# Kernel tuning notes

Hardware: AMD Instinct MI355X
Metric: run time of the kernel (lower is better)

The kernel has to match this reference:

```python
import jax, jax.numpy as jnp
import numpy as np

N_NODES = 100000
N_EDGES = 1600000
F_IN, HID, N_CLS = 128, 64, 40


def gcn_conv(x, src, dst, W, b, n_nodes):
    # x: [N, Fin] -> [N, Fout]; edges already include self-loops.
    h = x @ W  # [N, Fout]
    ones = jnp.ones_like(src, dtype=h.dtype)
    deg = jax.ops.segment_sum(ones, dst, num_segments=n_nodes)  # [N]
    dinv = jnp.where(deg > 0, jax.lax.rsqrt(deg), 0.0)
    norm = dinv[src] * dinv[dst]  # [E]
    msg = h[src] * norm[:, None]  # gather + scale
    out = jax.ops.segment_sum(msg, dst, num_segments=n_nodes)  # scatter-sum
    return out + b


def setup_inputs() -> dict:
    key = jax.random.key(0)
    ks = jax.random.split(key, 8)
    x = jax.random.normal(ks[0], (N_NODES, F_IN), dtype=jnp.float32)
    edge_index = jax.random.randint(ks[1], (2, N_EDGES), 0, N_NODES, dtype=jnp.int64)

    def glorot(k, fi, fo):
        s = float(np.sqrt(6.0 / (fi + fo)))
        return jax.random.uniform(k, (fi, fo), jnp.float32, -s, s)

    return {
        "x": x,
        "edge_index": edge_index,
        "W1": glorot(ks[2], F_IN, HID), "b1": jnp.zeros((HID,), jnp.float32),
        "W2": glorot(ks[3], HID, HID), "b2": jnp.zeros((HID,), jnp.float32),
        "W3": glorot(ks[4], HID, N_CLS), "b3": jnp.zeros((N_CLS,), jnp.float32),
    }


def reference(x, edge_index, W1, b1, W2, b2, W3, b3):
    n = x.shape[0]
    loop = jnp.arange(n, dtype=edge_index.dtype)
    src = jnp.concatenate([edge_index[0], loop])  # add self-loops
    dst = jnp.concatenate([edge_index[1], loop])
    # layer 1..3: GCNConv -> relu -> dropout(eval: identity)
    h = jax.nn.relu(gcn_conv(x, src, dst, W1, b1, n))
    h = jax.nn.relu(gcn_conv(h, src, dst, W2, b2, n))
    h = jax.nn.relu(gcn_conv(h, src, dst, W3, b3, n))
    return jax.nn.log_softmax(h, axis=1)
```

## Files before the change

### kernel.cpp

```cpp
#include <hip/hip_runtime.h>
#include <math.h>

typedef _Float16 half8   __attribute__((ext_vector_type(8)));
typedef float    float4v __attribute__((ext_vector_type(4)));

#define CAP   6144
#define EPB   8192

static __device__ __forceinline__ unsigned short f32_to_f16u(float f) {
    _Float16 h = (_Float16)f;
    return __builtin_bit_cast(unsigned short, h);
}


static __device__ __forceinline__ void prep_body(
    const float* __restrict__ W, unsigned short* __restrict__ Wf, int K, int M)
{
    const int NT = (M + 15) >> 4, NTC = NT << 4, KS = K >> 5;
    for (int i = threadIdx.x; i < K * NTC; i += 256) {
        int k = i / NTC, nn = i - k * NTC;
        unsigned short hv = 0;
        if (nn < M) hv = f32_to_f16u(W[(size_t)k * M + nn]);
        int s = k >> 5, q = (k >> 3) & 3, j = k & 7;
        int u = nn >> 4, lane = (q << 4) | (nn & 15);
        Wf[((u * KS + s) << 9) + (lane << 3) + j] = hv;
    }
}

template<int KK, int NT, int STRIDE, int MOUT, bool INF32, bool SCALE>
static __device__ __forceinline__ void gemm_body(
    unsigned short* __restrict__ ldsA, const void* __restrict__ Xin,
    const unsigned short* __restrict__ Wf, const float* __restrict__ dinv,
    unsigned short* __restrict__ H, int n, int bid)
{
    constexpr int KS = KK >> 5;
    const int tid = threadIdx.x;
    const int n0  = bid * 64;
    const int wv   = tid >> 6;
    const int lane = tid & 63;

    half8 bf[NT * KS];
    #pragma unroll
    for (int u = 0; u < NT; ++u)
        #pragma unroll
        for (int s = 0; s < KS; ++s)
            bf[u * KS + s] = *(const half8*)&Wf[((u * KS + s) << 9) + (lane << 3)];

    {
        const int rl = tid >> 3;
        const int kl = tid & 7;
        #pragma unroll
        for (int rb = 0; rb < 64; rb += 32) {
            int r = rl + rb;
            int node = n0 + r;
            int t = r >> 4, m = r & 15;
            if (INF32) {
                #pragma unroll
                for (int kq8 = 0; kq8 < (KK >> 2); kq8 += 8) {
                    int k0 = (kl + kq8) << 2;
                    unsigned short h[4] = {0, 0, 0, 0};
                    if (node < n) {
                        const float* xp = (const float*)Xin + (size_t)node * KK + k0;
                        float4v v = *(const float4v*)xp;
                        #pragma unroll
                        for (int i = 0; i < 4; ++i) h[i] = f32_to_f16u(v[i]);
                    }
                    int s = k0 >> 5, q = (k0 >> 3) & 3, j0 = k0 & 7;
                    int lds_lane = (q << 4) | m;
                    unsigned short* p = &ldsA[((t * KS + s) << 9) + (lds_lane << 3) + j0];
                    *(uint2*)p = make_uint2((unsigned)h[0] | ((unsigned)h[1] << 16),
                                            (unsigned)h[2] | ((unsigned)h[3] << 16));
                }
            } else {
                uint4 v = make_uint4(0, 0, 0, 0);
                if (node < n)
                    v = *(const uint4*)((const unsigned short*)Xin + (size_t)node * KK + (kl << 3));
                int k0 = kl << 3;
                int s = k0 >> 5, q = (k0 >> 3) & 3;
                unsigned short* p = &ldsA[((t * KS + s) << 9) + ((((q << 4) | m)) << 3)];
                *(uint4*)p = v;
            }
        }
    }

    __syncthreads();

    float4v acc[NT];
    #pragma unroll
    for (int u = 0; u < NT; ++u) acc[u] = (float4v){0.f, 0.f, 0.f, 0.f};

    #pragma unroll
    for (int s = 0; s < KS; ++s) {
        half8 a = *(const half8*)&ldsA[((wv * KS + s) << 9) + (lane << 3)];
        #pragma unroll
        for (int u = 0; u < NT; ++u)
            acc[u] = __builtin_amdgcn_mfma_f32_16x16x32_f16(a, bf[u * KS + s], acc[u], 0, 0, 0);
    }

    const int mc = lane & 15;
    const int quad = lane >> 4;
    #pragma unroll
    for (int reg = 0; reg < 4; ++reg) {
        int node = n0 + (wv << 4) + (quad << 2) + reg;
        if (node >= n) continue;
        float dv = SCALE ? dinv[node] : 1.0f;
        #pragma unroll
        for (int u = 0; u < NT; ++u) {
            int col = (u << 4) + mc;
            if (col < MOUT)
                H[(size_t)node * STRIDE + col] = f32_to_f16u(SCALE ? acc[u][reg] * dv
                                                                   : acc[u][reg]);
        }
    }
}

struct CsrS {
    int cnt[256]; int sc[256]; int cur[256];
    unsigned int pin[CAP]; int pout[CAP];
};

static __device__ __forceinline__ void csr_body(
    CsrS& S, const unsigned int* __restrict__ bint, const int* __restrict__ bcur,
    int2* __restrict__ rp2, float* __restrict__ dinv, int* __restrict__ es,
    int n, int b)
{
    const int tid = threadIdx.x;
    int total = bcur[b]; if (total > CAP) total = CAP;
    const unsigned int* bp = bint + (size_t)b * CAP;
    int* ep = es + (size_t)b * CAP;
    const int base = b * CAP;

    S.cnt[tid] = 0;
    __syncthreads();
    for (int i = tid; i < total; i += 256) {
        unsigned int v = bp[i];
        S.pin[i] = v;
        atomicAdd(&S.cnt[v & 255], 1);
    }
    __syncthreads();

    int v = S.cnt[tid];
    S.sc[tid] = v;
    __syncthreads();
    for (int off = 1; off < 256; off <<= 1) {
        int x = (tid >= off) ? S.sc[tid - off] : 0;
        __syncthreads();
        S.sc[tid] += x;
        __syncthreads();
    }
    int excl = S.sc[tid] - v;
    int node = (b << 8) + tid;
    if (node < n) {
        rp2[node]  = make_int2(base + excl, base + excl + v);
        dinv[node] = rsqrtf((float)(v + 1));
    }
    S.cur[tid] = excl;
    __syncthreads();

    for (int i = tid; i < total; i += 256) {
        unsigned int p = S.pin[i];
        int r = atomicAdd(&S.cur[p & 255], 1);
        S.pout[r] = (int)(p >> 8);
    }
    __syncthreads();

    for (int i = tid; i < total; i += 256)
        ep[i] = S.pout[i];
}


__global__ __launch_bounds__(256) void bin_prep(
    const int* __restrict__ src, const int* __restrict__ dst,
    int* __restrict__ bcur, unsigned int* __restrict__ bint, int E, int NB, int EB,
    const float* __restrict__ W1, const float* __restrict__ W2, const float* __restrict__ W3,
    unsigned short* __restrict__ Wf1, unsigned short* __restrict__ Wf2,
    unsigned short* __restrict__ Wf3)
{
    __shared__ unsigned int pay[EPB];
    __shared__ unsigned int targ[EPB];
    __shared__ int h[512];
    __shared__ int h2[512];
    __shared__ int sc[512];
    __shared__ int rbase[512];

    const int bx = (int)blockIdx.x;
    if (bx >= EB) {
        int k = bx - EB;
        if (k == 0)      prep_body(W1, Wf1, 128, 64);
        else if (k == 1) prep_body(W2, Wf2, 64, 64);
        else             prep_body(W3, Wf3, 64, 40);
        return;
    }

    const int tid  = threadIdx.x;
    const int base = bx * EPB;
    int end = base + EPB; if (end > E) end = E;
    const int total = end - base;
    const int L4 = total & ~3;

    h[tid] = 0; h[tid + 256] = 0;
    h2[tid] = 0; h2[tid + 256] = 0;
    __syncthreads();

    for (int i = tid << 2; i < L4; i += 1024) {
        int4 d4 = *(const int4*)(dst + base + i);
        atomicAdd(&h[d4.x >> 8], 1);
        atomicAdd(&h[d4.y >> 8], 1);
        atomicAdd(&h[d4.z >> 8], 1);
        atomicAdd(&h[d4.w >> 8], 1);
    }
    for (int i = L4 + tid; i < total; i += 256)
        atomicAdd(&h[dst[base + i] >> 8], 1);
    __syncthreads();

    int v0 = h[tid], v1 = h[tid + 256];
    sc[tid] = v0; sc[tid + 256] = v1;
    __syncthreads();
    for (int off = 1; off < 512; off <<= 1) {
        int x0 = (tid >= off) ? sc[tid - off] : 0;
        int x1 = (tid + 256 >= off) ? sc[tid + 256 - off] : 0;
        __syncthreads();
        sc[tid] += x0; sc[tid + 256] += x1;
        __syncthreads();
    }

    for (int j = tid; j < NB; j += 256) {
        int c = h[j];
        rbase[j] = c ? atomicAdd(&bcur[j], c) : 0;
    }
    __syncthreads();

    {
        auto place = [&](int d, int s) {
            int bkt  = d >> 8;
            int rank = atomicAdd(&h2[bkt], 1);
            int loc  = sc[bkt] - h[bkt] + rank;
            pay[loc] = ((unsigned int)s << 8) | (unsigned int)(d & 255);
            unsigned int t = (unsigned int)(rbase[bkt] + rank);
            targ[loc] = (t < (unsigned int)CAP)
                      ? (unsigned int)bkt * CAP + t : 0xFFFFFFFFu;
        };
        for (int i = tid << 2; i < L4; i += 1024) {
            int4 d4 = *(const int4*)(dst + base + i);
            int4 s4 = *(const int4*)(src + base + i);
            place(d4.x, s4.x); place(d4.y, s4.y);
            place(d4.z, s4.z); place(d4.w, s4.w);
        }
        for (int i = L4 + tid; i < total; i += 256)
            place(dst[base + i], src[base + i]);
    }
    __syncthreads();

    for (int i = tid; i < total; i += 256) {
        unsigned int t = targ[i];
        if (t != 0xFFFFFFFFu) bint[t] = pay[i];
    }
}


union SmemU {
    CsrS csr;
    unsigned short ldsA[4 * 4 * 512];
};

__global__ __launch_bounds__(256) void csr_gemm1(
    const unsigned int* __restrict__ bint, const int* __restrict__ bcur,
    int2* __restrict__ rp2, float* __restrict__ dinv, int* __restrict__ es,
    const float* __restrict__ x, const unsigned short* __restrict__ Wf1,
    unsigned short* __restrict__ H1, int n, int NBb)
{
    __shared__ __align__(16) SmemU sm;
    const int bx = (int)blockIdx.x;
    if (bx < NBb)
        csr_body(sm.csr, bint, bcur, rp2, dinv, es, n, bx);
    else
        gemm_body<128, 4, 64, 64, true, false>(sm.ldsA, x, Wf1, nullptr, H1, n, bx - NBb);
}


template<int KK, int NT, int STRIDE, int MOUT>
__global__ __launch_bounds__(256) void gemm_t(
    const void* __restrict__ Xin, const unsigned short* __restrict__ Wf,
    const float* __restrict__ dinv, unsigned short* __restrict__ H, int n)
{
    constexpr int KS = KK >> 5;
    __shared__ __align__(16) unsigned short ldsA[4 * KS * 512];
    gemm_body<KK, NT, STRIDE, MOUT, false, true>(ldsA, Xin, Wf, dinv, H, n, blockIdx.x);
}


template<int MOUT, int ROWU4, bool SRCSCALE>
__global__ __launch_bounds__(256) void gather_t(
    const int2* __restrict__ rp2, const int* __restrict__ es,
    const unsigned short* __restrict__ H, const float* __restrict__ dinv,
    const float* __restrict__ bias, unsigned short* __restrict__ Aout, int n)
{
    const int lane   = threadIdx.x & 63;
    const int half   = lane >> 5;
    const int lane32 = lane & 31;
    const int slot   = (lane >> 3) & 3;
    const int c8     = lane & 7;
    const bool act   = c8 < ROWU4;
    const uint4* H4  = (const uint4*)H;

    float bi[8];
    #pragma unroll
    for (int i = 0; i < 8; ++i) bi[i] = bias[(c8 << 3) + i];

    const half8 hz = {(_Float16)0, (_Float16)0, (_Float16)0, (_Float16)0,
                      (_Float16)0, (_Float16)0, (_Float16)0, (_Float16)0};

    const int TW2 = (int)(gridDim.x << 3);
    for (int nb = (((int)blockIdx.x << 2) + ((int)threadIdx.x >> 6)) << 1; nb < n; nb += TW2) {
        const int node = nb + half;
        const int2 e = rp2[node];
        const float dv = dinv[node];

        half8 hacc = hz;
        half8 self = hz;
        if (slot == 0 && act) {
            self = __builtin_bit_cast(half8, H4[(size_t)node * ROWU4 + c8]);
            if (!SRCSCALE) hacc = self;
        }

        for (int cb = e.x; cb < e.y; cb += 32) {
            const int rem = e.y - cb;
            int eidx = cb + lane32; if (eidx > e.y - 1) eidx = e.y - 1;
            const int ei = es[eidx];
            #pragma unroll
            for (int j = 0; j < 8; ++j) {
                const int idx = (j << 2) + slot;
                const int s = __shfl(ei, (half << 5) + idx, 64);
                if (idx < rem && act) {
                    half8 row = __builtin_bit_cast(half8, H4[(size_t)s * ROWU4 + c8]);
                    if (SRCSCALE) {
                        _Float16 dh = (_Float16)dinv[s];
                        half8 ds = {dh, dh, dh, dh, dh, dh, dh, dh};
                        hacc = hacc + ds * row;
                    } else {
                        hacc = hacc + row;
                    }
                }
            }
        }

        #pragma unroll
        for (int step = 8; step <= 16; step <<= 1) {
            uint4 u = __builtin_bit_cast(uint4, hacc);
            uint4 o;
            o.x = __shfl_xor(u.x, step, 64);
            o.y = __shfl_xor(u.y, step, 64);
            o.z = __shfl_xor(u.z, step, 64);
            o.w = __shfl_xor(u.w, step, 64);
            hacc = hacc + __builtin_bit_cast(half8, o);
        }

        if (slot == 0) {
            unsigned short o[8];
            #pragma unroll
            for (int i = 0; i < 8; ++i) {
                float a = SRCSCALE ? ((float)hacc[i] + (float)self[i] * dv) * dv
                                   : (float)hacc[i] * dv;
                o[i] = f32_to_f16u(fmaxf(a + bi[i], 0.0f));
            }
            uint4 w;
            w.x = (unsigned int)o[0] | ((unsigned int)o[1] << 16);
            w.y = (unsigned int)o[2] | ((unsigned int)o[3] << 16);
            w.z = (unsigned int)o[4] | ((unsigned int)o[5] << 16);
            w.w = (unsigned int)o[6] | ((unsigned int)o[7] << 16);
            ((uint4*)Aout)[(size_t)node * 8 + c8] = w;
        }
    }
}


template<int MOUT, int ROWU4>
__global__ __launch_bounds__(256) void gather_softmax(
    const int2* __restrict__ rp2, const int* __restrict__ es,
    const unsigned short* __restrict__ H, const float* __restrict__ dinv,
    const float* __restrict__ bias, float* __restrict__ out, int n)
{
    const int lane   = threadIdx.x & 63;
    const int half   = lane >> 5;
    const int lane32 = lane & 31;
    const int slot   = (lane >> 3) & 3;
    const int c8     = lane & 7;
    const bool act   = c8 < ROWU4;
    const uint4* H4  = (const uint4*)H;

    float bi[8];
    #pragma unroll
    for (int i = 0; i < 8; ++i) {
        int col = (c8 << 3) + i;
        bi[i] = (col < MOUT) ? bias[col] : 0.0f;
    }

    const half8 hz = {(_Float16)0, (_Float16)0, (_Float16)0, (_Float16)0,
                      (_Float16)0, (_Float16)0, (_Float16)0, (_Float16)0};

    const int TW2 = (int)(gridDim.x << 3);
    for (int nb = (((int)blockIdx.x << 2) + ((int)threadIdx.x >> 6)) << 1; nb < n; nb += TW2) {
        const int node = nb + half;
        const int2 e = rp2[node];
        const float dv = dinv[node];

        half8 hacc = hz;
        if (slot == 0 && act)
            hacc = __builtin_bit_cast(half8, H4[(size_t)node * ROWU4 + c8]);

        for (int cb = e.x; cb < e.y; cb += 32) {
            const int rem = e.y - cb;
            int eidx = cb + lane32; if (eidx > e.y - 1) eidx = e.y - 1;
            const int ei = es[eidx];
            #pragma unroll
            for (int j = 0; j < 8; ++j) {
                const int idx = (j << 2) + slot;
                const int s = __shfl(ei, (half << 5) + idx, 64);
                if (idx < rem && act)
                    hacc = hacc + __builtin_bit_cast(half8, H4[(size_t)s * ROWU4 + c8]);
            }
        }

        #pragma unroll
        for (int step = 8; step <= 16; step <<= 1) {
            uint4 u = __builtin_bit_cast(uint4, hacc);
            uint4 o;
            o.x = __shfl_xor(u.x, step, 64);
            o.y = __shfl_xor(u.y, step, 64);
            o.z = __shfl_xor(u.z, step, 64);
            o.w = __shfl_xor(u.w, step, 64);
            hacc = hacc + __builtin_bit_cast(half8, o);
        }

        float z[8]; float m = -INFINITY;
        #pragma unroll
        for (int i = 0; i < 8; ++i) {
            int col = (c8 << 3) + i;
            z[i] = (col < MOUT && act) ? fmaxf((float)hacc[i] * dv + bi[i], 0.0f)
                                       : -INFINITY;
            m = fmaxf(m, z[i]);
        }
        m = fmaxf(m, __shfl_xor(m, 1, 64));
        m = fmaxf(m, __shfl_xor(m, 2, 64));
        m = fmaxf(m, __shfl_xor(m, 4, 64));
        float s = 0.0f;
        #pragma unroll
        for (int i = 0; i < 8; ++i) s += expf(z[i] - m);
        s += __shfl_xor(s, 1, 64);
        s += __shfl_xor(s, 2, 64);
        s += __shfl_xor(s, 4, 64);
        float ls = logf(s) + m;
        if (slot == 0 && c8 < (MOUT + 7) / 8) {
            float* op = out + (size_t)node * MOUT + (c8 << 3);
            float4v o0 = {z[0] - ls, z[1] - ls, z[2] - ls, z[3] - ls};
            float4v o1 = {z[4] - ls, z[5] - ls, z[6] - ls, z[7] - ls};
            *(float4v*)op = o0;
            *(float4v*)(op + 4) = o1;
        }
    }
}


extern "C" void kernel_launch(void* const* d_in, const int* in_sizes, int n_in,
                              void* d_out, int out_size, void* d_ws, size_t ws_size,
                              hipStream_t stream)
{
    const float* x  = (const float*)d_in[0];
    const int*   ei = (const int*)  d_in[1];
    const float* W1 = (const float*)d_in[2];
    const float* b1 = (const float*)d_in[3];
    const float* W2 = (const float*)d_in[4];
    const float* b2 = (const float*)d_in[5];
    const float* W3 = (const float*)d_in[6];
    const float* b3 = (const float*)d_in[7];

    const int F_IN = 128;
    const int n = in_sizes[0] / F_IN;
    const int E = in_sizes[1] / 2;
    const int* src = ei;
    const int* dst = ei + E;
    float* out = (float*)d_out;

    const int NB = (n + 255) >> 8;

    auto align = [](size_t v) { return (v + 255) & ~(size_t)255; };
    char* w = (char*)d_ws;
    size_t off = 0;
    float*          dinv = (float*)(w + off);          off = align(off + (size_t)n * 4);
    unsigned short* H1   = (unsigned short*)(w + off); off = align(off + (size_t)n * 64 * 2);
    unsigned short* A    = (unsigned short*)(w + off); off = align(off + (size_t)n * 64 * 2);
    unsigned short* H3   = (unsigned short*)(w + off); off = align(off + (size_t)n * 40 * 2);
    int2*           rp2  = (int2*)(w + off);           off = align(off + (size_t)n * 8);
    int*            es   = (int*)(w + off);            off = align(off + (size_t)NB * CAP * 4);
    unsigned int*   bint = (unsigned int*)(w + off);   off = align(off + (size_t)NB * CAP * 4);
    int*            bcur = (int*)(w + off);            off = align(off + (size_t)512 * 4);
    unsigned short* Wf1  = (unsigned short*)(w + off); off = align(off + (size_t)8192 * 2);
    unsigned short* Wf2  = (unsigned short*)(w + off); off = align(off + (size_t)4096 * 2);
    unsigned short* Wf3  = (unsigned short*)(w + off); off = align(off + (size_t)3072 * 2);
    unsigned short* H2   = H1;

    const int BLK = 256;
    auto cdiv = [](int a, int b) { return (a + b - 1) / b; };
    const int EB = cdiv(E, EPB);
    const int GB = cdiv(n, 64);
    const int GG = 2048;

    hipMemsetAsync(bcur, 0, (size_t)512 * 4, stream);
    bin_prep<<<EB + 3, BLK, 0, stream>>>(src, dst, bcur, bint, E, NB, EB,
                                         W1, W2, W3, Wf1, Wf2, Wf3);

    csr_gemm1<<<NB + GB, BLK, 0, stream>>>(bint, bcur, rp2, dinv, es, x, Wf1, H1, n, NB);

    gather_t<64, 8, true><<<GG, BLK, 0, stream>>>(rp2, es, H1, dinv, b1, A, n);

    gemm_t<64, 4, 64, 64><<<GB, BLK, 0, stream>>>(A, Wf2, dinv, H2, n);
    gather_t<64, 8, false><<<GG, BLK, 0, stream>>>(rp2, es, H2, dinv, b2, A, n);

    gemm_t<64, 3, 40, 40><<<GB, BLK, 0, stream>>>(A, Wf3, dinv, H3, n);
    gather_softmax<40, 5><<<GG, BLK, 0, stream>>>(rp2, es, H3, dinv, b3, out, n);
}
```

Measured before the change: 250.2 us.

## Widen CSR buckets to 512 nodes and halve edges per binning block

Node buckets for the two-pass CSR build grow from 256 to 512 destination nodes, which halves the bucket count and the per-bucket global atomics. Each binning block now handles 4096 edges instead of 8192, giving more blocks in flight. The CSR build no longer stages the input in shared memory and re-reads it from global on the second pass, so its LDS footprint shrinks. The risks are more CSR work per block (512 nodes, up to 9216 edges) and fewer CSR blocks. Packing 9 bits of destination leaves 23 bits for the source index, enough for 100k nodes.

```diff
diff --git a/kernel.cpp b/kernel.cpp
--- a/kernel.cpp
+++ b/kernel.cpp
@@ -4,8 +4,9 @@
 typedef _Float16 half8   __attribute__((ext_vector_type(8)));
 typedef float    float4v __attribute__((ext_vector_type(4)));
 
-#define CAP   6144
-#define EPB   8192
+#define NPB   512
+#define CAP   9216
+#define EPB   4096
 
 static __device__ __forceinline__ unsigned short f32_to_f16u(float f) {
     _Float16 h = (_Float16)f;
@@ -115,8 +116,8 @@
 }
 
 struct CsrS {
-    int cnt[256]; int sc[256]; int cur[256];
-    unsigned int pin[CAP]; int pout[CAP];
+    int cnt[512]; int sc[512]; int cur[512];
+    int pout[CAP];
 };
 
 static __device__ __forceinline__ void csr_body(
@@ -130,37 +131,43 @@
     int* ep = es + (size_t)b * CAP;
     const int base = b * CAP;
 
-    S.cnt[tid] = 0;
-    __syncthreads();
+    S.cnt[tid] = 0; S.cnt[tid + 256] = 0;
+    __syncthreads();
+    for (int i = tid; i < total; i += 256)
+        atomicAdd(&S.cnt[bp[i] & 511], 1);
+    __syncthreads();
+
+    int v0 = S.cnt[tid], v1 = S.cnt[tid + 256];
+    S.sc[tid] = v0; S.sc[tid + 256] = v1;
+    __syncthreads();
+    for (int off = 1; off < 512; off <<= 1) {
+        int x0 = (tid >= off) ? S.sc[tid - off] : 0;
+        int x1 = (tid + 256 >= off) ? S.sc[tid + 256 - off] : 0;
+        __syncthreads();
+        S.sc[tid] += x0; S.sc[tid + 256] += x1;
+        __syncthreads();
+    }
+    {
+        int excl0 = S.sc[tid] - v0;
+        int excl1 = S.sc[tid + 256] - v1;
+        int node0 = (b << 9) + tid;
+        int node1 = node0 + 256;
+        if (node0 < n) {
+            rp2[node0]  = make_int2(base + excl0, base + excl0 + v0);
+            dinv[node0] = rsqrtf((float)(v0 + 1));
+        }
+        if (node1 < n) {
+            rp2[node1]  = make_int2(base + excl1, base + excl1 + v1);
+            dinv[node1] = rsqrtf((float)(v1 + 1));
+        }
+        S.cur[tid] = excl0; S.cur[tid + 256] = excl1;
+    }
+    __syncthreads();
+
     for (int i = tid; i < total; i += 256) {
-        unsigned int v = bp[i];
-        S.pin[i] = v;
-        atomicAdd(&S.cnt[v & 255], 1);
-    }
-    __syncthreads();
-
-    int v = S.cnt[tid];
-    S.sc[tid] = v;
-    __syncthreads();
-    for (int off = 1; off < 256; off <<= 1) {
-        int x = (tid >= off) ? S.sc[tid - off] : 0;
-        __syncthreads();
-        S.sc[tid] += x;
-        __syncthreads();
-    }
-    int excl = S.sc[tid] - v;
-    int node = (b << 8) + tid;
-    if (node < n) {
-        rp2[node]  = make_int2(base + excl, base + excl + v);
-        dinv[node] = rsqrtf((float)(v + 1));
-    }
-    S.cur[tid] = excl;
-    __syncthreads();
-
-    for (int i = tid; i < total; i += 256) {
-        unsigned int p = S.pin[i];
-        int r = atomicAdd(&S.cur[p & 255], 1);
-        S.pout[r] = (int)(p >> 8);
+        unsigned int p = bp[i];
+        int r = atomicAdd(&S.cur[p & 511], 1);
+        S.pout[r] = (int)(p >> 9);
     }
     __syncthreads();
 
@@ -178,10 +185,10 @@
 {
     __shared__ unsigned int pay[EPB];
     __shared__ unsigned int targ[EPB];
-    __shared__ int h[512];
-    __shared__ int h2[512];
-    __shared__ int sc[512];
-    __shared__ int rbase[512];
+    __shared__ int h[256];
+    __shared__ int h2[256];
+    __shared__ int sc[256];
+    __shared__ int rbase[256];
 
     const int bx = (int)blockIdx.x;
     if (bx >= EB) {
@@ -198,44 +205,42 @@
     const int total = end - base;
     const int L4 = total & ~3;
 
-    h[tid] = 0; h[tid + 256] = 0;
-    h2[tid] = 0; h2[tid + 256] = 0;
+    h[tid] = 0; h2[tid] = 0;
     __syncthreads();
 
     for (int i = tid << 2; i < L4; i += 1024) {
         int4 d4 = *(const int4*)(dst + base + i);
-        atomicAdd(&h[d4.x >> 8], 1);
-        atomicAdd(&h[d4.y >> 8], 1);
-        atomicAdd(&h[d4.z >> 8], 1);
-        atomicAdd(&h[d4.w >> 8], 1);
+        atomicAdd(&h[d4.x >> 9], 1);
+        atomicAdd(&h[d4.y >> 9], 1);
+        atomicAdd(&h[d4.z >> 9], 1);
+        atomicAdd(&h[d4.w >> 9], 1);
     }
     for (int i = L4 + tid; i < total; i += 256)
-        atomicAdd(&h[dst[base + i] >> 8], 1);
-    __syncthreads();
-
-    int v0 = h[tid], v1 = h[tid + 256];
-    sc[tid] = v0; sc[tid + 256] = v1;
-    __syncthreads();
-    for (int off = 1; off < 512; off <<= 1) {
-        int x0 = (tid >= off) ? sc[tid - off] : 0;
-        int x1 = (tid + 256 >= off) ? sc[tid + 256 - off] : 0;
+        atomicAdd(&h[dst[base + i] >> 9], 1);
+    __syncthreads();
+
+    int v = h[tid];
+    sc[tid] = v;
+    __syncthreads();
+    for (int off = 1; off < 256; off <<= 1) {
+        int x = (tid >= off) ? sc[tid - off] : 0;
         __syncthreads();
-        sc[tid] += x0; sc[tid + 256] += x1;
+        sc[tid] += x;
         __syncthreads();
     }
 
-    for (int j = tid; j < NB; j += 256) {
-        int c = h[j];
-        rbase[j] = c ? atomicAdd(&bcur[j], c) : 0;
+    if (tid < NB) {
+        int c = h[tid];
+        rbase[tid] = c ? atomicAdd(&bcur[tid], c) : 0;
     }
     __syncthreads();
 
     {
         auto place = [&](int d, int s) {
-            int bkt  = d >> 8;
+            int bkt  = d >> 9;
             int rank = atomicAdd(&h2[bkt], 1);
             int loc  = sc[bkt] - h[bkt] + rank;
-            pay[loc] = ((unsigned int)s << 8) | (unsigned int)(d & 255);
+            pay[loc] = ((unsigned int)s << 9) | (unsigned int)(d & 511);
             unsigned int t = (unsigned int)(rbase[bkt] + rank);
             targ[loc] = (t < (unsigned int)CAP)
                       ? (unsigned int)bkt * CAP + t : 0xFFFFFFFFu;
@@ -481,7 +486,7 @@
     const int* dst = ei + E;
     float* out = (float*)d_out;
 
-    const int NB = (n + 255) >> 8;
+    const int NB = (n + NPB - 1) / NPB;
 
     auto align = [](size_t v) { return (v + 255) & ~(size_t)255; };
     char* w = (char*)d_ws;
```

Measured after the change: 255.6 us. 1.02x slower.

## Split gather/GEMM by node halves to overlap second-half gather with first-half GEMM

Applied to the files above, without the earlier changes.

Each gather+GEMM layer pair is split into node halves. A mixed kernel runs the gather for the second half of the nodes alongside the GEMM for the first half, whose gather finished in an earlier launch. A final GEMM launch then handles the remaining rows. This aims to fill idle compute units during the memory-bound gather and hide the GEMM, at the cost of more kernel launches and an extra H2 buffer so the GEMM output does not alias its input.

```diff
diff --git a/kernel.cpp b/kernel.cpp
--- a/kernel.cpp
+++ b/kernel.cpp
@@ -168,132 +168,12 @@
         ep[i] = S.pout[i];
 }
 
-
-__global__ __launch_bounds__(256) void bin_prep(
-    const int* __restrict__ src, const int* __restrict__ dst,
-    int* __restrict__ bcur, unsigned int* __restrict__ bint, int E, int NB, int EB,
-    const float* __restrict__ W1, const float* __restrict__ W2, const float* __restrict__ W3,
-    unsigned short* __restrict__ Wf1, unsigned short* __restrict__ Wf2,
-    unsigned short* __restrict__ Wf3)
-{
-    __shared__ unsigned int pay[EPB];
-    __shared__ unsigned int targ[EPB];
-    __shared__ int h[512];
-    __shared__ int h2[512];
-    __shared__ int sc[512];
-    __shared__ int rbase[512];
-
-    const int bx = (int)blockIdx.x;
-    if (bx >= EB) {
-        int k = bx - EB;
-        if (k == 0)      prep_body(W1, Wf1, 128, 64);
-        else if (k == 1) prep_body(W2, Wf2, 64, 64);
-        else             prep_body(W3, Wf3, 64, 40);
-        return;
-    }
-
-    const int tid  = threadIdx.x;
-    const int base = bx * EPB;
-    int end = base + EPB; if (end > E) end = E;
-    const int total = end - base;
-    const int L4 = total & ~3;
-
-    h[tid] = 0; h[tid + 256] = 0;
-    h2[tid] = 0; h2[tid + 256] = 0;
-    __syncthreads();
-
-    for (int i = tid << 2; i < L4; i += 1024) {
-        int4 d4 = *(const int4*)(dst + base + i);
-        atomicAdd(&h[d4.x >> 8], 1);
-        atomicAdd(&h[d4.y >> 8], 1);
-        atomicAdd(&h[d4.z >> 8], 1);
-        atomicAdd(&h[d4.w >> 8], 1);
-    }
-    for (int i = L4 + tid; i < total; i += 256)
-        atomicAdd(&h[dst[base + i] >> 8], 1);
-    __syncthreads();
-
-    int v0 = h[tid], v1 = h[tid + 256];
-    sc[tid] = v0; sc[tid + 256] = v1;
-    __syncthreads();
-    for (int off = 1; off < 512; off <<= 1) {
-        int x0 = (tid >= off) ? sc[tid - off] : 0;
-        int x1 = (tid + 256 >= off) ? sc[tid + 256 - off] : 0;
-        __syncthreads();
-        sc[tid] += x0; sc[tid + 256] += x1;
-        __syncthreads();
-    }
-
-    for (int j = tid; j < NB; j += 256) {
-        int c = h[j];
-        rbase[j] = c ? atomicAdd(&bcur[j], c) : 0;
-    }
-    __syncthreads();
-
-    {
-        auto place = [&](int d, int s) {
-            int bkt  = d >> 8;
-            int rank = atomicAdd(&h2[bkt], 1);
-            int loc  = sc[bkt] - h[bkt] + rank;
-            pay[loc] = ((unsigned int)s << 8) | (unsigned int)(d & 255);
-            unsigned int t = (unsigned int)(rbase[bkt] + rank);
-            targ[loc] = (t < (unsigned int)CAP)
-                      ? (unsigned int)bkt * CAP + t : 0xFFFFFFFFu;
-        };
-        for (int i = tid << 2; i < L4; i += 1024) {
-            int4 d4 = *(const int4*)(dst + base + i);
-            int4 s4 = *(const int4*)(src + base + i);
-            place(d4.x, s4.x); place(d4.y, s4.y);
-            place(d4.z, s4.z); place(d4.w, s4.w);
-        }
-        for (int i = L4 + tid; i < total; i += 256)
-            place(dst[base + i], src[base + i]);
-    }
-    __syncthreads();
-
-    for (int i = tid; i < total; i += 256) {
-        unsigned int t = targ[i];
-        if (t != 0xFFFFFFFFu) bint[t] = pay[i];
-    }
-}
-
-
-union SmemU {
-    CsrS csr;
-    unsigned short ldsA[4 * 4 * 512];
-};
-
-__global__ __launch_bounds__(256) void csr_gemm1(
-    const unsigned int* __restrict__ bint, const int* __restrict__ bcur,
-    int2* __restrict__ rp2, float* __restrict__ dinv, int* __restrict__ es,
-    const float* __restrict__ x, const unsigned short* __restrict__ Wf1,
-    unsigned short* __restrict__ H1, int n, int NBb)
-{
-    __shared__ __align__(16) SmemU sm;
-    const int bx = (int)blockIdx.x;
-    if (bx < NBb)
-        csr_body(sm.csr, bint, bcur, rp2, dinv, es, n, bx);
-    else
-        gemm_body<128, 4, 64, 64, true, false>(sm.ldsA, x, Wf1, nullptr, H1, n, bx - NBb);
-}
-
-
-template<int KK, int NT, int STRIDE, int MOUT>
-__global__ __launch_bounds__(256) void gemm_t(
-    const void* __restrict__ Xin, const unsigned short* __restrict__ Wf,
-    const float* __restrict__ dinv, unsigned short* __restrict__ H, int n)
-{
-    constexpr int KS = KK >> 5;
-    __shared__ __align__(16) unsigned short ldsA[4 * KS * 512];
-    gemm_body<KK, NT, STRIDE, MOUT, false, true>(ldsA, Xin, Wf, dinv, H, n, blockIdx.x);
-}
-
-
 template<int MOUT, int ROWU4, bool SRCSCALE>
-__global__ __launch_bounds__(256) void gather_t(
+static __device__ __forceinline__ void gather_body(
     const int2* __restrict__ rp2, const int* __restrict__ es,
     const unsigned short* __restrict__ H, const float* __restrict__ dinv,
-    const float* __restrict__ bias, unsigned short* __restrict__ Aout, int n)
+    const float* __restrict__ bias, unsigned short* __restrict__ Aout,
+    int n0, int n1, int nblk, int bid)
 {
     const int lane   = threadIdx.x & 63;
     const int half   = lane >> 5;
@@ -310,8 +190,8 @@
     const half8 hz = {(_Float16)0, (_Float16)0, (_Float16)0, (_Float16)0,
                       (_Float16)0, (_Float16)0, (_Float16)0, (_Float16)0};
 
-    const int TW2 = (int)(gridDim.x << 3);
-    for (int nb = (((int)blockIdx.x << 2) + ((int)threadIdx.x >> 6)) << 1; nb < n; nb += TW2) {
+    const int TW2 = nblk << 3;
+    for (int nb = n0 + (((bid << 2) + ((int)threadIdx.x >> 6)) << 1); nb < n1; nb += TW2) {
         const int node = nb + half;
         const int2 e = rp2[node];
         const float dv = dinv[node];
@@ -374,6 +254,155 @@
 }
 
 
+__global__ __launch_bounds__(256) void bin_prep(
+    const int* __restrict__ src, const int* __restrict__ dst,
+    int* __restrict__ bcur, unsigned int* __restrict__ bint, int E, int NB, int EB,
+    const float* __restrict__ W1, const float* __restrict__ W2, const float* __restrict__ W3,
+    unsigned short* __restrict__ Wf1, unsigned short* __restrict__ Wf2,
+    unsigned short* __restrict__ Wf3)
+{
+    __shared__ unsigned int pay[EPB];
+    __shared__ unsigned int targ[EPB];
+    __shared__ int h[512];
+    __shared__ int h2[512];
+    __shared__ int sc[512];
+    __shared__ int rbase[512];
+
+    const int bx = (int)blockIdx.x;
+    if (bx >= EB) {
+        int k = bx - EB;
+        if (k == 0)      prep_body(W1, Wf1, 128, 64);
+        else if (k == 1) prep_body(W2, Wf2, 64, 64);
+        else             prep_body(W3, Wf3, 64, 40);
+        return;
+    }
+
+    const int tid  = threadIdx.x;
+    const int base = bx * EPB;
+    int end = base + EPB; if (end > E) end = E;
+    const int total = end - base;
+    const int L4 = total & ~3;
+
+    h[tid] = 0; h[tid + 256] = 0;
+    h2[tid] = 0; h2[tid + 256] = 0;
+    __syncthreads();
+
+    for (int i = tid << 2; i < L4; i += 1024) {
+        int4 d4 = *(const int4*)(dst + base + i);
+        atomicAdd(&h[d4.x >> 8], 1);
+        atomicAdd(&h[d4.y >> 8], 1);
+        atomicAdd(&h[d4.z >> 8], 1);
+        atomicAdd(&h[d4.w >> 8], 1);
+    }
+    for (int i = L4 + tid; i < total; i += 256)
+        atomicAdd(&h[dst[base + i] >> 8], 1);
+    __syncthreads();
+
+    int v0 = h[tid], v1 = h[tid + 256];
+    sc[tid] = v0; sc[tid + 256] = v1;
+    __syncthreads();
+    for (int off = 1; off < 512; off <<= 1) {
+        int x0 = (tid >= off) ? sc[tid - off] : 0;
+        int x1 = (tid + 256 >= off) ? sc[tid + 256 - off] : 0;
+        __syncthreads();
+        sc[tid] += x0; sc[tid + 256] += x1;
+        __syncthreads();
+    }
+
+    for (int j = tid; j < NB; j += 256) {
+        int c = h[j];
+        rbase[j] = c ? atomicAdd(&bcur[j], c) : 0;
+    }
+    __syncthreads();
+
+    {
+        auto place = [&](int d, int s) {
+            int bkt  = d >> 8;
+            int rank = atomicAdd(&h2[bkt], 1);
+            int loc  = sc[bkt] - h[bkt] + rank;
+            pay[loc] = ((unsigned int)s << 8) | (unsigned int)(d & 255);
+            unsigned int t = (unsigned int)(rbase[bkt] + rank);
+            targ[loc] = (t < (unsigned int)CAP)
+                      ? (unsigned int)bkt * CAP + t : 0xFFFFFFFFu;
+        };
+        for (int i = tid << 2; i < L4; i += 1024) {
+            int4 d4 = *(const int4*)(dst + base + i);
+            int4 s4 = *(const int4*)(src + base + i);
+            place(d4.x, s4.x); place(d4.y, s4.y);
+            place(d4.z, s4.z); place(d4.w, s4.w);
+        }
+        for (int i = L4 + tid; i < total; i += 256)
+            place(dst[base + i], src[base + i]);
+    }
+    __syncthreads();
+
+    for (int i = tid; i < total; i += 256) {
+        unsigned int t = targ[i];
+        if (t != 0xFFFFFFFFu) bint[t] = pay[i];
+    }
+}
+
+
+union SmemU {
+    CsrS csr;
+    unsigned short ldsA[4 * 4 * 512];
+};
+
+__global__ __launch_bounds__(256) void csr_gemm1(
+    const unsigned int* __restrict__ bint, const int* __restrict__ bcur,
+    int2* __restrict__ rp2, float* __restrict__ dinv, int* __restrict__ es,
+    const float* __restrict__ x, const unsigned short* __restrict__ Wf1,
+    unsigned short* __restrict__ H1, int n, int NBb)
+{
+    __shared__ __align__(16) SmemU sm;
+    const int bx = (int)blockIdx.x;
+    if (bx < NBb)
+        csr_body(sm.csr, bint, bcur, rp2, dinv, es, n, bx);
+    else
+        gemm_body<128, 4, 64, 64, true, false>(sm.ldsA, x, Wf1, nullptr, H1, n, bx - NBb);
+}
+
+
+template<int KK, int NT, int STRIDE, int MOUT>
+__global__ __launch_bounds__(256) void gemm_t(
+    const void* __restrict__ Xin, const unsigned short* __restrict__ Wf,
+    const float* __restrict__ dinv, unsigned short* __restrict__ H, int n, int bid0)
+{
+    constexpr int KS = KK >> 5;
+    __shared__ __align__(16) unsigned short ldsA[4 * KS * 512];
+    gemm_body<KK, NT, STRIDE, MOUT, false, true>(ldsA, Xin, Wf, dinv, H, n, (int)blockIdx.x + bid0);
+}
+
+template<int MOUT, int ROWU4, bool SRCSCALE>
+__global__ __launch_bounds__(256) void gather_t(
+    const int2* __restrict__ rp2, const int* __restrict__ es,
+    const unsigned short* __restrict__ H, const float* __restrict__ dinv,
+    const float* __restrict__ bias, unsigned short* __restrict__ Aout, int n0, int n1)
+{
+    gather_body<MOUT, ROWU4, SRCSCALE>(rp2, es, H, dinv, bias, Aout,
+                                       n0, n1, (int)gridDim.x, (int)blockIdx.x);
+}
+
+
+template<bool SRCSCALE, int GNT, int GSTRIDE, int GMOUT>
+__global__ __launch_bounds__(256) void gather_gemm_mix(
+    const int2* __restrict__ rp2, const int* __restrict__ es,
+    const unsigned short* __restrict__ Hin, const float* __restrict__ dinv,
+    const float* __restrict__ bias, unsigned short* __restrict__ Aout,
+    int gn0, int gn1, int GGM,
+    const unsigned short* __restrict__ Xin, const unsigned short* __restrict__ Wf,
+    unsigned short* __restrict__ Hout, int glim)
+{
+    __shared__ __align__(16) unsigned short ldsA[4 * 2 * 512];
+    const int bx = (int)blockIdx.x;
+    if (bx < GGM)
+        gather_body<64, 8, SRCSCALE>(rp2, es, Hin, dinv, bias, Aout, gn0, gn1, GGM, bx);
+    else
+        gemm_body<64, GNT, GSTRIDE, GMOUT, false, true>(ldsA, Xin, Wf, dinv, Hout, glim,
+                                                        bx - GGM);
+}
+
+
 template<int MOUT, int ROWU4>
 __global__ __launch_bounds__(256) void gather_softmax(
     const int2* __restrict__ rp2, const int* __restrict__ es,
@@ -488,8 +517,8 @@
     size_t off = 0;
     float*          dinv = (float*)(w + off);          off = align(off + (size_t)n * 4);
     unsigned short* H1   = (unsigned short*)(w + off); off = align(off + (size_t)n * 64 * 2);
+    unsigned short* H2   = (unsigned short*)(w + off); off = align(off + (size_t)n * 64 * 2);
     unsigned short* A    = (unsigned short*)(w + off); off = align(off + (size_t)n * 64 * 2);
-    unsigned short* H3   = (unsigned short*)(w + off); off = align(off + (size_t)n * 40 * 2);
     int2*           rp2  = (int2*)(w + off);           off = align(off + (size_t)n * 8);
     int*            es   = (int*)(w + off);            off = align(off + (size_t)NB * CAP * 4);
     unsigned int*   bint = (unsigned int*)(w + off);   off = align(off + (size_t)NB * CAP * 4);
@@ -497,13 +526,17 @@
     unsigned short* Wf1  = (unsigned short*)(w + off); off = align(off + (size_t)8192 * 2);
     unsigned short* Wf2  = (unsigned short*)(w + off); off = align(off + (size_t)4096 * 2);
     unsigned short* Wf3  = (unsigned short*)(w + off); off = align(off + (size_t)3072 * 2);
-    unsigned short* H2   = H1;
+    unsigned short* H3   = H1;
 
     const int BLK = 256;
     auto cdiv = [](int a, int b) { return (a + b - 1) / b; };
-    const int EB = cdiv(E, EPB);
-    const int GB = cdiv(n, 64);
-    const int GG = 2048;
+    const int EB  = cdiv(E, EPB);
+    const int GB  = cdiv(n, 64);
+    const int NH  = cdiv(n / 2, 64) * 64;
+    const int GBH = NH / 64;
+    const int GBR = GB - GBH;
+    const int GGA = 1024;
+    const int GG  = 2048;
 
     hipMemsetAsync(bcur, 0, (size_t)512 * 4, stream);
     bin_prep<<<EB + 3, BLK, 0, stream>>>(src, dst, bcur, bint, E, NB, EB,
@@ -511,11 +544,15 @@
 
     csr_gemm1<<<NB + GB, BLK, 0, stream>>>(bint, bcur, rp2, dinv, es, x, Wf1, H1, n, NB);
 
-    gather_t<64, 8, true><<<GG, BLK, 0, stream>>>(rp2, es, H1, dinv, b1, A, n);
-
-    gemm_t<64, 4, 64, 64><<<GB, BLK, 0, stream>>>(A, Wf2, dinv, H2, n);
-    gather_t<64, 8, false><<<GG, BLK, 0, stream>>>(rp2, es, H2, dinv, b2, A, n);
-
-    gemm_t<64, 3, 40, 40><<<GB, BLK, 0, stream>>>(A, Wf3, dinv, H3, n);
+    gather_t<64, 8, true><<<GGA, BLK, 0, stream>>>(rp2, es, H1, dinv, b1, A, 0, NH);
+    gather_gemm_mix<true, 4, 64, 64><<<GGA + GBH, BLK, 0, stream>>>(
+        rp2, es, H1, dinv, b1, A, NH, n, GGA, A, Wf2, H2, NH);
+    gemm_t<64, 4, 64, 64><<<GBR, BLK, 0, stream>>>(A, Wf2, dinv, H2, n, GBH);
+
+    gather_t<64, 8, false><<<GGA, BLK, 0, stream>>>(rp2, es, H2, dinv, b2, A, 0, NH);
+    gather_gemm_mix<false, 3, 40, 40><<<GGA + GBH, BLK, 0, stream>>>(
+        rp2, es, H2, dinv, b2, A, NH, n, GGA, A, Wf3, H3, NH);
+    gemm_t<64, 3, 40, 40><<<GBR, BLK, 0, stream>>>(A, Wf3, dinv, H3, n, GBH);
+
     gather_softmax<40, 5><<<GG, BLK, 0, stream>>>(rp2, es, H3, dinv, b3, out, n);
 }
```

New measurement: 277.5 us. 10.9% more time.
